# Performance work log

Hardware: AMD Instinct MI355X
Metric: run time of the kernel (lower is better)

Reference implementation:

```python
import jax, jax.numpy as jnp
import numpy as np

B, C_ENT, C_REL = 32768, 1000, 500


def setup_inputs() -> dict:
    key = jax.random.key(0)
    ks = jax.random.split(key, 6)
    return {
        "sub_input": jax.random.normal(ks[0], (B, C_ENT), dtype=jnp.float32),
        "relation_input": jax.random.normal(ks[1], (B, C_REL), dtype=jnp.float32),
        "obj_input": jax.random.normal(ks[2], (B, C_ENT), dtype=jnp.float32),
        "sub_target": jax.random.randint(ks[3], (B,), 0, C_ENT, dtype=jnp.int32),
        "relation_target": jax.random.randint(ks[4], (B,), 0, C_REL, dtype=jnp.int32),
        "obj_target": jax.random.randint(ks[5], (B,), 0, C_ENT, dtype=jnp.int32),
    }


def reference(sub_input, relation_input, obj_input, sub_target, relation_target, obj_target):
    s = jax.nn.softmax(sub_input, axis=1)
    r = jax.nn.softmax(relation_input, axis=1)
    o = jax.nn.softmax(obj_input, axis=1)
    b = s.shape[0]
    rows = jnp.arange(b)

    # ground-truth triplet probability
    gt = s[rows, sub_target] * r[rows, relation_target] * o[rows, obj_target]

    # top-2 values/indices per row (replaces full torch.sort)
    sv, si = jax.lax.top_k(s, 2)
    rv, ri = jax.lax.top_k(r, 2)
    ov, oi = jax.lax.top_k(o, 2)

    # all three argmaxes match the targets?
    cond = (si[:, 0] == sub_target) & (ri[:, 0] == relation_target) & (oi[:, 0] == obj_target)

    # 8 combinations of top-2 probs; second-smallest of the 8 (torch.sort ascending, index 1)
    tmp = (sv[:, :, None, None] * rv[:, None, :, None] * ov[:, None, None, :]).reshape(b, 8)
    second_smallest = jnp.sort(tmp, axis=1)[:, 1]

    top1 = sv[:, 0] * rv[:, 0] * ov[:, 0]
    pre = jnp.where(cond, second_smallest, top1)

    out = 1.0 - gt + pre
    return jnp.mean(jnp.maximum(out, 0.0))
```

## Files before the change

### kernel.cpp

```cpp
#include <hip/hip_runtime.h>
#include <float.h>


constexpr int B      = 32768;
constexpr int C_ENT  = 1000;
constexpr int C_REL  = 500;

__device__ inline void combine_stats(float& m1, int& i1, float& m2, float& Z,
                                     float bm1, int bi1, float bm2, float bZ) {
  bool bwin = (bm1 > m1) || (bm1 == m1 && bi1 < i1);
  float wm1 = bwin ? bm1 : m1;
  int   wi1 = bwin ? bi1 : i1;
  float wm2 = bwin ? bm2 : m2;
  float lm1 = bwin ? m1  : bm1;
  float wZ  = bwin ? bZ  : Z;
  float lZ  = bwin ? Z   : bZ;
  m1 = wm1;
  i1 = wi1;
  m2 = fmaxf(wm2, lm1);
  Z  = wZ + lZ * __expf(lm1 - wm1);
}

template<int NK, int C4>
__device__ inline void row_stats(const float* __restrict__ row, int lane, int target,
                                 float& p_top1, float& p_top2, int& amax, float& p_tgt) {
  const float4* row4 = (const float4*)row;
  float4 v[NK];
#pragma unroll
  for (int k = 0; k < NK; ++k) {
    int idx = lane + 64 * k;
    if (idx < C4) v[k] = row4[idx];
    else          v[k] = make_float4(-FLT_MAX, -FLT_MAX, -FLT_MAX, -FLT_MAX);
  }
  float m1 = -FLT_MAX, m2 = -FLT_MAX;
  int   i1 = 0x7fffffff;
#pragma unroll
  for (int k = 0; k < NK; ++k) {
    int base = 4 * (lane + 64 * k);
    float a0 = v[k].x, a1 = v[k].y, a2 = v[k].z, a3 = v[k].w;
    if (a0 > m1) { m2 = m1; m1 = a0; i1 = base;     } else if (a0 > m2) m2 = a0;
    if (a1 > m1) { m2 = m1; m1 = a1; i1 = base + 1; } else if (a1 > m2) m2 = a1;
    if (a2 > m1) { m2 = m1; m1 = a2; i1 = base + 2; } else if (a2 > m2) m2 = a2;
    if (a3 > m1) { m2 = m1; m1 = a3; i1 = base + 3; } else if (a3 > m2) m2 = a3;
  }
  float Z = 0.f;
#pragma unroll
  for (int k = 0; k < NK; ++k) {
    Z += __expf(v[k].x - m1);
    Z += __expf(v[k].y - m1);
    Z += __expf(v[k].z - m1);
    Z += __expf(v[k].w - m1);
  }
#pragma unroll
  for (int off = 32; off > 0; off >>= 1) {
    float bm1 = __shfl_xor(m1, off);
    int   bi1 = __shfl_xor(i1, off);
    float bm2 = __shfl_xor(m2, off);
    float bZ  = __shfl_xor(Z,  off);
    combine_stats(m1, i1, m2, Z, bm1, bi1, bm2, bZ);
  }
  float invZ = 1.0f / Z;
  float xt   = row[target];
  p_top1 = invZ;
  p_top2 = __expf(m2 - m1) * invZ;
  p_tgt  = __expf(xt - m1) * invZ;
  amax   = i1;
}

template<bool ATOMIC>
__global__ __launch_bounds__(256) void rank_loss_kernel(
    const float* __restrict__ s, const float* __restrict__ r, const float* __restrict__ o,
    const int* __restrict__ st, const int* __restrict__ rt, const int* __restrict__ ot,
    float* __restrict__ partial, float* __restrict__ out) {
  const int wid  = threadIdx.x >> 6;
  const int lane = threadIdx.x & 63;
  const int row  = blockIdx.x * 4 + wid;

  const float* srow = s + (size_t)row * C_ENT;
  const float* rrow = r + (size_t)row * C_REL;
  const float* orow = o + (size_t)row * C_ENT;
  const int tS = st[row], tR = rt[row], tO = ot[row];

  float sp0, sp1, spt; int sa;
  float rp0, rp1, rpt; int ra;
  float op0, op1, opt; int oa;
  row_stats<4, C_ENT / 4>(srow, lane, tS, sp0, sp1, sa, spt);
  row_stats<2, C_REL / 4>(rrow, lane, tR, rp0, rp1, ra, rpt);
  row_stats<4, C_ENT / 4>(orow, lane, tO, op0, op1, oa, opt);

  if (lane == 0) {
    float gt   = spt * rpt * opt;
    float top1 = sp0 * rp0 * op0;
    float c1 = sp0 * rp1 * op1;
    float c2 = sp1 * rp0 * op1;
    float c3 = sp1 * rp1 * op0;
    float second = fminf(c1, fminf(c2, c3));
    bool cond = (sa == tS) && (ra == tR) && (oa == tO);
    float pre = cond ? second : top1;
    float val = fmaxf(1.0f - gt + pre, 0.0f);
    if (ATOMIC) atomicAdd(out, val * (1.0f / (float)B));
    else        partial[row] = val;
  }
}

__global__ __launch_bounds__(1024) void reduce_sum_kernel(const float* __restrict__ p,
                                                          float* __restrict__ out) {
  const float4* p4 = (const float4*)p;
  float sum = 0.f;
  for (int i = threadIdx.x; i < B / 4; i += 1024) {
    float4 v = p4[i];
    sum += (v.x + v.y) + (v.z + v.w);
  }
#pragma unroll
  for (int off = 32; off > 0; off >>= 1) sum += __shfl_xor(sum, off);
  __shared__ float lds[16];
  if ((threadIdx.x & 63) == 0) lds[threadIdx.x >> 6] = sum;
  __syncthreads();
  if (threadIdx.x == 0) {
    float t = 0.f;
#pragma unroll
    for (int i = 0; i < 16; ++i) t += lds[i];
    out[0] = t * (1.0f / (float)B);
  }
}

extern "C" void kernel_launch(void* const* d_in, const int* in_sizes, int n_in,
                              void* d_out, int out_size, void* d_ws, size_t ws_size,
                              hipStream_t stream) {
  const float* s  = (const float*)d_in[0];
  const float* r  = (const float*)d_in[1];
  const float* o  = (const float*)d_in[2];
  const int*   st = (const int*)d_in[3];
  const int*   rt = (const int*)d_in[4];
  const int*   ot = (const int*)d_in[5];
  float* out = (float*)d_out;

  if (ws_size >= (size_t)B * sizeof(float)) {
    float* partial = (float*)d_ws;
    rank_loss_kernel<false><<<B / 4, 256, 0, stream>>>(s, r, o, st, rt, ot, partial, nullptr);
    reduce_sum_kernel<<<1, 1024, 0, stream>>>(partial, out);
  } else {
    hipMemsetAsync(d_out, 0, sizeof(float), stream);
    rank_loss_kernel<true><<<B / 4, 256, 0, stream>>>(s, r, o, st, rt, ot, nullptr, out);
  }
}
```

Before: 320.7 us.

## Split per-row stats into one wave per matrix row plus combine kernel

Each wave now handles a single row of one of the three input matrices, so the grid has three times as many waves. Per-row softmax stats go to a workspace buffer, and a separate kernel combines them into the per-row loss. The row reduction also changes: a max butterfly runs first, then one pass computes the sum of exponentials, the second maximum, the argmax index and a tie count, replacing the sequential top-2 logic and the exp-rescaling combine. This aims for more memory-level parallelism and less serial work per wave, at the cost of an extra launch, workspace traffic, and possibly unbalanced waves since relation rows are half the length.

```diff
diff --git a/kernel.cpp b/kernel.cpp
--- a/kernel.cpp
+++ b/kernel.cpp
@@ -1,10 +1,107 @@
 #include <hip/hip_runtime.h>
 #include <float.h>
+#include <limits.h>
 
 
 constexpr int B      = 32768;
 constexpr int C_ENT  = 1000;
 constexpr int C_REL  = 500;
+
+
+template<int NK, int C4>
+__device__ inline float4 wave_stats(const float* __restrict__ row, int lane, int target) {
+  const float4* row4 = (const float4*)row;
+  float4 v[NK];
+#pragma unroll
+  for (int k = 0; k < NK; ++k) {
+    int i = lane + 64 * k;
+    v[k] = (i < C4) ? row4[i] : make_float4(-FLT_MAX, -FLT_MAX, -FLT_MAX, -FLT_MAX);
+  }
+  float xt = row[target];
+
+  float lm = -FLT_MAX;
+#pragma unroll
+  for (int k = 0; k < NK; ++k)
+    lm = fmaxf(lm, fmaxf(fmaxf(v[k].x, v[k].y), fmaxf(v[k].z, v[k].w)));
+#pragma unroll
+  for (int off = 32; off; off >>= 1)
+    lm = fmaxf(lm, __shfl_xor(lm, off));
+  const float m1 = lm;
+
+  float z[NK];
+  float m2 = -FLT_MAX;
+  int   idx = INT_MAX;
+  int   cnt = 0;
+#pragma unroll
+  for (int k = 0; k < NK; ++k) {
+    const int base = 4 * (lane + 64 * k);
+    const float a0 = v[k].x, a1 = v[k].y, a2 = v[k].z, a3 = v[k].w;
+    z[k] = (__expf(a0 - m1) + __expf(a1 - m1)) + (__expf(a2 - m1) + __expf(a3 - m1));
+    const bool e0 = (a0 == m1), e1 = (a1 == m1), e2 = (a2 == m1), e3 = (a3 == m1);
+    cnt += (int)e0 + (int)e1 + (int)e2 + (int)e3;
+    m2 = fmaxf(m2, fmaxf(e0 ? -FLT_MAX : a0, e1 ? -FLT_MAX : a1));
+    m2 = fmaxf(m2, fmaxf(e2 ? -FLT_MAX : a2, e3 ? -FLT_MAX : a3));
+    const int i01 = min(e0 ? base     : INT_MAX, e1 ? base + 1 : INT_MAX);
+    const int i23 = min(e2 ? base + 2 : INT_MAX, e3 ? base + 3 : INT_MAX);
+    idx = min(idx, min(i01, i23));
+  }
+  float Z;
+  if constexpr (NK == 4) Z = (z[0] + z[1]) + (z[2] + z[3]);
+  else                   Z = z[0] + z[1];
+
+#pragma unroll
+  for (int off = 32; off; off >>= 1) {
+    Z   += __shfl_xor(Z, off);
+    m2   = fmaxf(m2, __shfl_xor(m2, off));
+    cnt += __shfl_xor(cnt, off);
+    idx  = min(idx, __shfl_xor(idx, off));
+  }
+  if (cnt >= 2) m2 = m1;
+
+  const float invZ = 1.0f / Z;
+  return make_float4(invZ,
+                     __expf(m2 - m1) * invZ,
+                     __expf(xt - m1) * invZ,
+                     __int_as_float(idx));
+}
+
+__global__ __launch_bounds__(256) void stats_kernel(
+    const float* __restrict__ s, const float* __restrict__ r, const float* __restrict__ o,
+    const int* __restrict__ st, const int* __restrict__ rt, const int* __restrict__ ot,
+    float4* __restrict__ out4) {
+  const int wid  = threadIdx.x >> 6;
+  const int lane = threadIdx.x & 63;
+  const int gw   = blockIdx.x * 4 + wid;
+  const int m    = gw >> 15;
+  const int row  = gw & (B - 1);
+  float4 res;
+  if (m == 0)      res = wave_stats<4, C_ENT / 4>(s + (size_t)row * C_ENT, lane, st[row]);
+  else if (m == 1) res = wave_stats<4, C_ENT / 4>(o + (size_t)row * C_ENT, lane, ot[row]);
+  else             res = wave_stats<2, C_REL / 4>(r + (size_t)row * C_REL, lane, rt[row]);
+  if (lane == 0) out4[m * B + row] = res;
+}
+
+__global__ __launch_bounds__(256) void combine_kernel(
+    const float4* __restrict__ stat4,
+    const int* __restrict__ st, const int* __restrict__ rt, const int* __restrict__ ot,
+    float* __restrict__ partial) {
+  const int row = blockIdx.x * 256 + threadIdx.x;
+  const float4 S = stat4[row];
+  const float4 O = stat4[B + row];
+  const float4 R = stat4[2 * B + row];
+  const float gt   = S.z * R.z * O.z;
+  const float top1 = S.x * R.x * O.x;
+  const float c1 = S.x * R.y * O.y;
+  const float c2 = S.y * R.x * O.y;
+  const float c3 = S.y * R.y * O.x;
+  const float second = fminf(c1, fminf(c2, c3));
+  const bool cond = (__float_as_int(S.w) == st[row]) &&
+                    (__float_as_int(R.w) == rt[row]) &&
+                    (__float_as_int(O.w) == ot[row]);
+  const float pre = cond ? second : top1;
+  partial[row] = fmaxf(1.0f - gt + pre, 0.0f);
+}
+
 
 __device__ inline void combine_stats(float& m1, int& i1, float& m2, float& Z,
                                      float bm1, int bi1, float bm2, float bZ) {
@@ -15,8 +112,7 @@
   float lm1 = bwin ? m1  : bm1;
   float wZ  = bwin ? bZ  : Z;
   float lZ  = bwin ? Z   : bZ;
-  m1 = wm1;
-  i1 = wi1;
+  m1 = wm1; i1 = wi1;
   m2 = fmaxf(wm2, lm1);
   Z  = wZ + lZ * __expf(lm1 - wm1);
 }
@@ -29,8 +125,7 @@
 #pragma unroll
   for (int k = 0; k < NK; ++k) {
     int idx = lane + 64 * k;
-    if (idx < C4) v[k] = row4[idx];
-    else          v[k] = make_float4(-FLT_MAX, -FLT_MAX, -FLT_MAX, -FLT_MAX);
+    v[k] = (idx < C4) ? row4[idx] : make_float4(-FLT_MAX, -FLT_MAX, -FLT_MAX, -FLT_MAX);
   }
   float m1 = -FLT_MAX, m2 = -FLT_MAX;
   int   i1 = 0x7fffffff;
@@ -46,10 +141,8 @@
   float Z = 0.f;
 #pragma unroll
   for (int k = 0; k < NK; ++k) {
-    Z += __expf(v[k].x - m1);
-    Z += __expf(v[k].y - m1);
-    Z += __expf(v[k].z - m1);
-    Z += __expf(v[k].w - m1);
+    Z += __expf(v[k].x - m1); Z += __expf(v[k].y - m1);
+    Z += __expf(v[k].z - m1); Z += __expf(v[k].w - m1);
   }
 #pragma unroll
   for (int off = 32; off > 0; off >>= 1) {
@@ -103,6 +196,7 @@
   }
 }
 
+
 __global__ __launch_bounds__(1024) void reduce_sum_kernel(const float* __restrict__ p,
                                                           float* __restrict__ out) {
   const float4* p4 = (const float4*)p;
@@ -135,7 +229,14 @@
   const int*   ot = (const int*)d_in[5];
   float* out = (float*)d_out;
 
-  if (ws_size >= (size_t)B * sizeof(float)) {
+  const size_t statBytes = (size_t)3 * B * sizeof(float4);
+  if (ws_size >= statBytes + (size_t)B * sizeof(float)) {
+    float4* stat4  = (float4*)d_ws;
+    float* partial = (float*)((char*)d_ws + statBytes);
+    stats_kernel<<<3 * B / 4, 256, 0, stream>>>(s, r, o, st, rt, ot, stat4);
+    combine_kernel<<<B / 256, 256, 0, stream>>>(stat4, st, rt, ot, partial);
+    reduce_sum_kernel<<<1, 1024, 0, stream>>>(partial, out);
+  } else if (ws_size >= (size_t)B * sizeof(float)) {
     float* partial = (float*)d_ws;
     rank_loss_kernel<false><<<B / 4, 256, 0, stream>>>(s, r, o, st, rt, ot, partial, nullptr);
     reduce_sum_kernel<<<1, 1024, 0, stream>>>(partial, out);
```

Measured after the change: 319.4 us. About the same (-0.4%).

## Split rows into 500-float units with software-pipelined per-wave stats and combine pass

Applied to the files above, without the earlier changes.

Rows are split into uniform 500-element units (two halves per entity row, one per relation row). Each wave processes 16 units and prefetches upcoming units while computing the current one, using a single-pass max, exp2-based partition sum and duplicate-aware second max. A second kernel merges the half-row stats, computes the loss per row and reduces with block shuffles plus one atomic per block. This is meant to raise memory-level parallelism and balance work across waves. The cost is an extra workspace round trip and a memset launch.

```diff
diff --git a/kernel.cpp b/kernel.cpp
--- a/kernel.cpp
+++ b/kernel.cpp
@@ -1,10 +1,161 @@
 #include <hip/hip_runtime.h>
 #include <float.h>
-
-
-constexpr int B      = 32768;
-constexpr int C_ENT  = 1000;
-constexpr int C_REL  = 500;
+#include <limits.h>
+
+
+constexpr int B     = 32768;
+constexpr int C_ENT = 1000;
+constexpr int C_REL = 500;
+constexpr int NU    = 163840;
+constexpr int UPW   = 16;
+constexpr float LOG2E = 1.4426950408889634f;
+
+__device__ inline float fast_exp2(float x) { return exp2f(x); }
+
+__device__ inline const float4* unit_ptr(int u, const float* s, const float* r,
+                                         const float* o) {
+  const float* p;
+  if (u < 2 * B)        p = s + ((size_t)(u >> 1) * C_ENT + (size_t)(u & 1) * C_REL);
+  else if (u < 4 * B) { int v = u - 2 * B;
+                        p = o + ((size_t)(v >> 1) * C_ENT + (size_t)(v & 1) * C_REL); }
+  else                  p = r + (size_t)(u - 4 * B) * C_REL;
+  return (const float4*)p;
+}
+__device__ inline int unit_ioff(int u) { return (u < 4 * B) ? (u & 1) * C_REL : 0; }
+
+__device__ inline void unit_load(const float4* p4, int lane, float4& va, float4& vb) {
+  va = make_float4(-FLT_MAX, -FLT_MAX, -FLT_MAX, -FLT_MAX);
+  vb = va;
+  if (lane <= 62) va = p4[2 * lane];
+  if (lane <= 61) vb = p4[2 * lane + 1];
+}
+
+__device__ inline float4 unit_compute(const float4 va, const float4 vb,
+                                      int lane, int ioff) {
+  float m = fmaxf(fmaxf(fmaxf(va.x, va.y), fmaxf(va.z, va.w)),
+                  fmaxf(fmaxf(vb.x, vb.y), fmaxf(vb.z, vb.w)));
+#pragma unroll
+  for (int off = 32; off; off >>= 1) m = fmaxf(m, __shfl_xor(m, off));
+  const float m1 = m;
+  const float nm1l = -m1 * LOG2E;
+
+  float z = (fast_exp2(fmaf(va.x, LOG2E, nm1l)) + fast_exp2(fmaf(va.y, LOG2E, nm1l))) +
+            (fast_exp2(fmaf(va.z, LOG2E, nm1l)) + fast_exp2(fmaf(va.w, LOG2E, nm1l))) +
+            (fast_exp2(fmaf(vb.x, LOG2E, nm1l)) + fast_exp2(fmaf(vb.y, LOG2E, nm1l))) +
+            (fast_exp2(fmaf(vb.z, LOG2E, nm1l)) + fast_exp2(fmaf(vb.w, LOG2E, nm1l)));
+
+  const bool e0 = (va.x == m1), e1 = (va.y == m1), e2 = (va.z == m1), e3 = (va.w == m1);
+  const bool e4 = (vb.x == m1), e5 = (vb.y == m1), e6 = (vb.z == m1), e7 = (vb.w == m1);
+  const int cnt = ((int)e0 + (int)e1 + (int)e2 + (int)e3) +
+                  ((int)e4 + (int)e5 + (int)e6 + (int)e7);
+  float m2 = fmaxf(fmaxf(fmaxf(e0 ? -FLT_MAX : va.x, e1 ? -FLT_MAX : va.y),
+                         fmaxf(e2 ? -FLT_MAX : va.z, e3 ? -FLT_MAX : va.w)),
+                   fmaxf(fmaxf(e4 ? -FLT_MAX : vb.x, e5 ? -FLT_MAX : vb.y),
+                         fmaxf(e6 ? -FLT_MAX : vb.z, e7 ? -FLT_MAX : vb.w)));
+  const int li = e0 ? 0 : e1 ? 1 : e2 ? 2 : e3 ? 3 : e4 ? 4 : e5 ? 5 : e6 ? 6 : 7;
+
+  const unsigned long long b1 = __ballot(cnt >= 1);
+  const unsigned long long b2 = __ballot(cnt >= 2);
+  const bool dup = (__popcll(b1) >= 2) || (b2 != 0ULL);
+  const int src = __ffsll(b1) - 1;
+  const int gidx = ioff + 8 * src + __shfl(li, src);
+
+#pragma unroll
+  for (int off = 32; off; off >>= 1) {
+    z += __shfl_xor(z, off);
+    m2 = fmaxf(m2, __shfl_xor(m2, off));
+  }
+  if (dup) m2 = m1;
+
+  return make_float4(m1, m2, z, __int_as_float(gidx));
+}
+
+__global__ __launch_bounds__(256, 4) void stats_kernel(
+    const float* __restrict__ s, const float* __restrict__ r, const float* __restrict__ o,
+    float4* __restrict__ out4) {
+  const int lane = threadIdx.x & 63;
+  const int u0 = (blockIdx.x * 4 + (threadIdx.x >> 6)) * UPW;
+
+  float4 Aa, Ab, Ba, Bb, Ca, Cb, Da, Db;
+  unit_load(unit_ptr(u0 + 0, s, r, o), lane, Aa, Ab);
+  unit_load(unit_ptr(u0 + 1, s, r, o), lane, Ba, Bb);
+  unit_load(unit_ptr(u0 + 2, s, r, o), lane, Ca, Cb);
+
+#pragma unroll
+  for (int j = 0; j < UPW; j += 4) {
+    float4 res;
+    if (j + 3 < UPW) unit_load(unit_ptr(u0 + j + 3, s, r, o), lane, Da, Db);
+    res = unit_compute(Aa, Ab, lane, unit_ioff(u0 + j + 0));
+    if (lane == 0) out4[u0 + j + 0] = res;
+    if (j + 4 < UPW) unit_load(unit_ptr(u0 + j + 4, s, r, o), lane, Aa, Ab);
+    res = unit_compute(Ba, Bb, lane, unit_ioff(u0 + j + 1));
+    if (lane == 0) out4[u0 + j + 1] = res;
+    if (j + 5 < UPW) unit_load(unit_ptr(u0 + j + 5, s, r, o), lane, Ba, Bb);
+    res = unit_compute(Ca, Cb, lane, unit_ioff(u0 + j + 2));
+    if (lane == 0) out4[u0 + j + 2] = res;
+    if (j + 6 < UPW) unit_load(unit_ptr(u0 + j + 6, s, r, o), lane, Ca, Cb);
+    res = unit_compute(Da, Db, lane, unit_ioff(u0 + j + 3));
+    if (lane == 0) out4[u0 + j + 3] = res;
+  }
+}
+
+__device__ inline void merge_halves(float4 a, float4 b,
+                                    float& m1, float& m2, float& Z, int& idx) {
+  m1 = fmaxf(a.x, b.x);
+  Z  = a.z * fast_exp2((a.x - m1) * LOG2E) + b.z * fast_exp2((b.x - m1) * LOG2E);
+  m2 = fmaxf(fminf(a.x, b.x), (a.x >= b.x) ? a.y : b.y);
+  idx = (b.x > a.x) ? __float_as_int(b.w) : __float_as_int(a.w);
+}
+
+__global__ __launch_bounds__(256) void combine_kernel(
+    const float4* __restrict__ st4,
+    const float* __restrict__ s, const float* __restrict__ r, const float* __restrict__ o,
+    const int* __restrict__ st, const int* __restrict__ rt, const int* __restrict__ ot,
+    float* __restrict__ out) {
+  const int row = blockIdx.x * 256 + threadIdx.x;
+
+  const float4 sa = st4[2 * row],         sb = st4[2 * row + 1];
+  const float4 oa = st4[2 * B + 2 * row], ob = st4[2 * B + 2 * row + 1];
+  const float4 rr = st4[4 * B + row];
+  const int ts = st[row], tr = rt[row], to = ot[row];
+  const float xs = s[(size_t)row * C_ENT + ts];
+  const float xr = r[(size_t)row * C_REL + tr];
+  const float xo = o[(size_t)row * C_ENT + to];
+
+  float sm1, sm2, sZ; int si;
+  float om1, om2, oZ; int oi;
+  merge_halves(sa, sb, sm1, sm2, sZ, si);
+  merge_halves(oa, ob, om1, om2, oZ, oi);
+  const float rm1 = rr.x, rm2 = rr.y, rZ = rr.z;
+  const int ri = __float_as_int(rr.w);
+
+  const float sI = 1.0f / sZ, rI = 1.0f / rZ, oI = 1.0f / oZ;
+  const float sp1 = fast_exp2((sm2 - sm1) * LOG2E) * sI;
+  const float rp1 = fast_exp2((rm2 - rm1) * LOG2E) * rI;
+  const float op1 = fast_exp2((om2 - om1) * LOG2E) * oI;
+  const float spt = fast_exp2((xs - sm1) * LOG2E) * sI;
+  const float rpt = fast_exp2((xr - rm1) * LOG2E) * rI;
+  const float opt = fast_exp2((xo - om1) * LOG2E) * oI;
+
+  const float gt   = spt * rpt * opt;
+  const float top1 = sI * rI * oI;
+  const float c1 = sI  * rp1 * op1;
+  const float c2 = sp1 * rI  * op1;
+  const float c3 = sp1 * rp1 * oI;
+  const float second = fminf(c1, fminf(c2, c3));
+  const bool cond = (si == ts) && (ri == tr) && (oi == to);
+  const float pre = cond ? second : top1;
+  float val = fmaxf(1.0f - gt + pre, 0.0f) * (1.0f / (float)B);
+
+#pragma unroll
+  for (int off = 32; off; off >>= 1) val += __shfl_xor(val, off);
+  __shared__ float lds[4];
+  if ((threadIdx.x & 63) == 0) lds[threadIdx.x >> 6] = val;
+  __syncthreads();
+  if (threadIdx.x == 0)
+    atomicAdd(out, (lds[0] + lds[1]) + (lds[2] + lds[3]));
+}
+
 
 __device__ inline void combine_stats(float& m1, int& i1, float& m2, float& Z,
                                      float bm1, int bi1, float bm2, float bZ) {
@@ -15,8 +166,7 @@
   float lm1 = bwin ? m1  : bm1;
   float wZ  = bwin ? bZ  : Z;
   float lZ  = bwin ? Z   : bZ;
-  m1 = wm1;
-  i1 = wi1;
+  m1 = wm1; i1 = wi1;
   m2 = fmaxf(wm2, lm1);
   Z  = wZ + lZ * __expf(lm1 - wm1);
 }
@@ -29,8 +179,7 @@
 #pragma unroll
   for (int k = 0; k < NK; ++k) {
     int idx = lane + 64 * k;
-    if (idx < C4) v[k] = row4[idx];
-    else          v[k] = make_float4(-FLT_MAX, -FLT_MAX, -FLT_MAX, -FLT_MAX);
+    v[k] = (idx < C4) ? row4[idx] : make_float4(-FLT_MAX, -FLT_MAX, -FLT_MAX, -FLT_MAX);
   }
   float m1 = -FLT_MAX, m2 = -FLT_MAX;
   int   i1 = 0x7fffffff;
@@ -46,10 +195,8 @@
   float Z = 0.f;
 #pragma unroll
   for (int k = 0; k < NK; ++k) {
-    Z += __expf(v[k].x - m1);
-    Z += __expf(v[k].y - m1);
-    Z += __expf(v[k].z - m1);
-    Z += __expf(v[k].w - m1);
+    Z += __expf(v[k].x - m1); Z += __expf(v[k].y - m1);
+    Z += __expf(v[k].z - m1); Z += __expf(v[k].w - m1);
   }
 #pragma unroll
   for (int off = 32; off > 0; off >>= 1) {
@@ -67,26 +214,21 @@
   amax   = i1;
 }
 
-template<bool ATOMIC>
-__global__ __launch_bounds__(256) void rank_loss_kernel(
+__global__ __launch_bounds__(256) void rank_loss_atomic_kernel(
     const float* __restrict__ s, const float* __restrict__ r, const float* __restrict__ o,
     const int* __restrict__ st, const int* __restrict__ rt, const int* __restrict__ ot,
-    float* __restrict__ partial, float* __restrict__ out) {
+    float* __restrict__ out) {
   const int wid  = threadIdx.x >> 6;
   const int lane = threadIdx.x & 63;
   const int row  = blockIdx.x * 4 + wid;
 
-  const float* srow = s + (size_t)row * C_ENT;
-  const float* rrow = r + (size_t)row * C_REL;
-  const float* orow = o + (size_t)row * C_ENT;
   const int tS = st[row], tR = rt[row], tO = ot[row];
-
   float sp0, sp1, spt; int sa;
   float rp0, rp1, rpt; int ra;
   float op0, op1, opt; int oa;
-  row_stats<4, C_ENT / 4>(srow, lane, tS, sp0, sp1, sa, spt);
-  row_stats<2, C_REL / 4>(rrow, lane, tR, rp0, rp1, ra, rpt);
-  row_stats<4, C_ENT / 4>(orow, lane, tO, op0, op1, oa, opt);
+  row_stats<4, C_ENT / 4>(s + (size_t)row * C_ENT, lane, tS, sp0, sp1, sa, spt);
+  row_stats<2, C_REL / 4>(r + (size_t)row * C_REL, lane, tR, rp0, rp1, ra, rpt);
+  row_stats<4, C_ENT / 4>(o + (size_t)row * C_ENT, lane, tO, op0, op1, oa, opt);
 
   if (lane == 0) {
     float gt   = spt * rpt * opt;
@@ -97,30 +239,7 @@
     float second = fminf(c1, fminf(c2, c3));
     bool cond = (sa == tS) && (ra == tR) && (oa == tO);
     float pre = cond ? second : top1;
-    float val = fmaxf(1.0f - gt + pre, 0.0f);
-    if (ATOMIC) atomicAdd(out, val * (1.0f / (float)B));
-    else        partial[row] = val;
-  }
-}
-
-__global__ __launch_bounds__(1024) void reduce_sum_kernel(const float* __restrict__ p,
-                                                          float* __restrict__ out) {
-  const float4* p4 = (const float4*)p;
-  float sum = 0.f;
-  for (int i = threadIdx.x; i < B / 4; i += 1024) {
-    float4 v = p4[i];
-    sum += (v.x + v.y) + (v.z + v.w);
-  }
-#pragma unroll
-  for (int off = 32; off > 0; off >>= 1) sum += __shfl_xor(sum, off);
-  __shared__ float lds[16];
-  if ((threadIdx.x & 63) == 0) lds[threadIdx.x >> 6] = sum;
-  __syncthreads();
-  if (threadIdx.x == 0) {
-    float t = 0.f;
-#pragma unroll
-    for (int i = 0; i < 16; ++i) t += lds[i];
-    out[0] = t * (1.0f / (float)B);
+    atomicAdd(out, fmaxf(1.0f - gt + pre, 0.0f) * (1.0f / (float)B));
   }
 }
 
@@ -135,12 +254,12 @@
   const int*   ot = (const int*)d_in[5];
   float* out = (float*)d_out;
 
-  if (ws_size >= (size_t)B * sizeof(float)) {
-    float* partial = (float*)d_ws;
-    rank_loss_kernel<false><<<B / 4, 256, 0, stream>>>(s, r, o, st, rt, ot, partial, nullptr);
-    reduce_sum_kernel<<<1, 1024, 0, stream>>>(partial, out);
+  hipMemsetAsync(d_out, 0, sizeof(float), stream);
+  if (ws_size >= (size_t)NU * sizeof(float4)) {
+    float4* stat4 = (float4*)d_ws;
+    stats_kernel<<<NU / UPW / 4, 256, 0, stream>>>(s, r, o, stat4);
+    combine_kernel<<<B / 256, 256, 0, stream>>>(stat4, s, r, o, st, rt, ot, out);
   } else {
-    hipMemsetAsync(d_out, 0, sizeof(float), stream);
-    rank_loss_kernel<true><<<B / 4, 256, 0, stream>>>(s, r, o, st, rt, ot, nullptr, out);
-  }
-}
+    rank_loss_atomic_kernel<<<B / 4, 256, 0, stream>>>(s, r, o, st, rt, ot, out);
+  }
+}
```

New measurement: 336.0 us. 4.8% more time.
